# Optimization experiments

Hardware: AMD Instinct MI355X
Metric: run time of the kernel (lower is better)

Reference implementation:

```python
import jax, jax.numpy as jnp
import numpy as np

D_MODEL = 256
KSIZE = 16
EPS = 1e-5


def conv1d(x, w, b):
    # x: [B, C, N], w: [O, C, K], SAME padding over node axis
    y = jax.lax.conv_general_dilated(x, w, window_strides=(1,), padding='SAME',
                                     dimension_numbers=('NCH', 'OIH', 'NCH'))
    return y + b[None, :, None]


def layernorm(x, g, b):
    mu = jnp.mean(x, axis=-1, keepdims=True)
    var = jnp.mean(jnp.square(x - mu), axis=-1, keepdims=True)
    return (x - mu) * jax.lax.rsqrt(var + EPS) * g + b


def setup_inputs() -> dict:
    key = jax.random.key(0)
    ks = jax.random.split(key, 16)
    B, N, d, K = 4, 2048, D_MODEL, KSIZE
    conv_scale = 1.0 / np.sqrt(d * K)
    lin_scale = 1.0 / np.sqrt(d)
    return {
        'src': jax.random.normal(ks[0], (B, N, d), jnp.float32),
        'x_lst': jnp.zeros((B, N, N), jnp.float32),
        'adj': jax.random.randint(ks[1], (B, N, N), 0, 2, jnp.int32),
        'dis': jax.random.uniform(ks[2], (B, N, N), jnp.float32),
        'Wq': jax.random.normal(ks[3], (d, d, K), jnp.float32) * conv_scale,
        'bq': jnp.zeros((d,), jnp.float32),
        'Wk': jax.random.normal(ks[4], (d, d, K), jnp.float32) * conv_scale,
        'bk': jnp.zeros((d,), jnp.float32),
        'Wv': jax.random.normal(ks[5], (d, d, K), jnp.float32) * conv_scale,
        'bv': jnp.zeros((d,), jnp.float32),
        'W1': jax.random.normal(ks[6], (d, d), jnp.float32) * lin_scale,
        'b1': jnp.zeros((d,), jnp.float32),
        'W2': jax.random.normal(ks[7], (d, d), jnp.float32) * lin_scale,
        'b2': jnp.zeros((d,), jnp.float32),
        'W3': jax.random.normal(ks[8], (d, d), jnp.float32) * lin_scale,
        'b3': jnp.zeros((d,), jnp.float32),
        'g1': jnp.ones((d,), jnp.float32),
        'be1': jnp.zeros((d,), jnp.float32),
        'g2': jnp.ones((d,), jnp.float32),
        'be2': jnp.zeros((d,), jnp.float32),
    }


def reference(src, x_lst, adj, dis, Wq, bq, Wk, bk, Wv, bv,
              W1, b1, W2, b2, W3, b3, g1, be1, g2, be2):
    # ---- _ga_block: transpose to channel-major, graph attention ----
    x = jnp.swapaxes(src, -2, -1)                      # [B, d, N]
    q = conv1d(x, Wq, bq)                              # [B, d, N]
    k = conv1d(x, Wk, bk)
    v = conv1d(x, Wv, bv)
    scale = 1.0 / jnp.sqrt(jnp.asarray(D_MODEL, src.dtype))
    scores = jnp.einsum('bdn,bdm->bnm', q, k) * scale  # [B, N, N]
    scores = scores - dis                              # distance bias
    scores = jnp.where(adj > 0, scores, jnp.asarray(-1e9, scores.dtype))
    attn = jax.nn.softmax(scores, axis=-1)             # [B, N, N]
    x_lst_new = x_lst + attn                           # accumulated attention state
    out = jnp.einsum('bnm,bdm->bdn', attn, v)          # [B, d, N]
    x1 = jnp.swapaxes(out, -2, -1)                     # [B, N, d] (dropout = identity in eval)
    # ---- residual + norm1 ----
    h = layernorm(src + x1, g1, be1)
    # ---- 3-layer LeakyReLU MLP + residual + norm2 ----
    m = jax.nn.leaky_relu(h @ W1.T + b1)
    m = jax.nn.leaky_relu(m @ W2.T + b2)
    m = m @ W3.T + b3
    h = layernorm(h + m, g2, be2)
    return h, x_lst_new
```

## Files before the change

kernel.cpp:

```cpp
#include <hip/hip_runtime.h>
#include <stdint.h>

typedef _Float16 h16;
typedef _Float16 h8v __attribute__((ext_vector_type(8)));
typedef float    f4v __attribute__((ext_vector_type(4)));
typedef int      i4v __attribute__((ext_vector_type(4)));

#define NBATCH 4
#define NNODE  2048
#define DM     256
#define NPAD   2063

__device__ __forceinline__ void async16(const void* g, void* l) {
#if __has_builtin(__builtin_amdgcn_global_load_lds)
  __builtin_amdgcn_global_load_lds((__attribute__((address_space(1))) void*)g,
                                   (__attribute__((address_space(3))) void*)l, 16, 0, 0);
#else
  *(f4v*)l = *(const f4v*)g;
#endif
}

__device__ __forceinline__ void gemm_tile(
    const h16* Abase, int astride,
    const h16* Bbase, int bstride,
    h16* As, h16* Bs, f4v acc[4][4], int kiters)
{
  const int tid  = threadIdx.x;
  const int lane = tid & 63;
  const int wv   = tid >> 6;
  const int srow = tid >> 2;
  const int sch  = ((tid & 3) ^ ((tid >> 3) & 3)) * 8;
  const h16* gA0 = Abase + (long)srow * astride + sch;
  const h16* gA1 = Abase + (long)(srow + 64) * astride + sch;
  const h16* gB0 = Bbase + (long)srow * bstride + sch;
  const h16* gB1 = Bbase + (long)(srow + 64) * bstride + sch;
  h16* lA0 = As + tid * 8;
  h16* lA1 = As + 2048 + tid * 8;
  h16* lB0 = Bs + tid * 8;
  h16* lB1 = Bs + 2048 + tid * 8;
  const int swz = ((lane & 15) >> 1) & 3;
  const int qq  = ((lane >> 4) ^ swz) * 8;
  const int amr = ((wv & 1) * 64 + (lane & 15)) * 32 + qq;
  const int bnr = ((wv >> 1) * 64 + (lane & 15)) * 32 + qq;

  for (int kt = 0; kt < kiters; ++kt) {
    const int k0 = kt * 32;
    __syncthreads();
    async16(gA0 + k0, lA0);
    async16(gA1 + k0, lA1);
    async16(gB0 + k0, lB0);
    async16(gB1 + k0, lB1);
    asm volatile("s_waitcnt vmcnt(0)" ::: "memory");
    __syncthreads();
    h8v af[4], bf[4];
#pragma unroll
    for (int i = 0; i < 4; ++i) af[i] = *(const h8v*)(As + amr + i * (16 * 32));
#pragma unroll
    for (int j = 0; j < 4; ++j) bf[j] = *(const h8v*)(Bs + bnr + j * (16 * 32));
#pragma unroll
    for (int i = 0; i < 4; ++i)
#pragma unroll
      for (int j = 0; j < 4; ++j)
        acc[i][j] = __builtin_amdgcn_mfma_f32_16x16x32_f16(af[i], bf[j], acc[i][j], 0, 0, 0);
  }
}

__device__ __forceinline__ void zero_acc(f4v acc[4][4]) {
#pragma unroll
  for (int i = 0; i < 4; ++i)
#pragma unroll
    for (int j = 0; j < 4; ++j) {
      f4v z = {0.f, 0.f, 0.f, 0.f};
      acc[i][j] = z;
    }
}

__global__ void prep_src_kernel(const float* __restrict__ src, h16* __restrict__ Xpad) {
  int idx = blockIdx.x * 256 + threadIdx.x;
  int c = idx & 255;
  int row = idx >> 8;
  int b = row / NPAD;
  int n = row - b * NPAD;
  float v = 0.f;
  int ns = n - 7;
  if (ns >= 0 && ns < NNODE) v = src[((long)b * NNODE + ns) * DM + c];
  Xpad[idx] = (h16)v;
}

__global__ void prep_wconv_kernel(const float* __restrict__ Wq, const float* __restrict__ Wk,
                                  const float* __restrict__ Wv, h16* __restrict__ Wt) {
  int idx = blockIdx.x * 256 + threadIdx.x;
  int w = idx >> 20;
  int rem = idx & 1048575;
  int o = rem >> 12;
  int tc = rem & 4095;
  int t = tc >> 8;
  int c = tc & 255;
  const float* W = (w == 0) ? Wq : (w == 1) ? Wk : Wv;
  Wt[idx] = (h16)W[(o * 256 + c) * 16 + t];
}

__global__ void prep_wlin_kernel(const float* __restrict__ W1, const float* __restrict__ W2,
                                 const float* __restrict__ W3, h16* __restrict__ Wl) {
  int idx = blockIdx.x * 256 + threadIdx.x;
  int w = idx >> 16;
  int rem = idx & 65535;
  const float* W = (w == 0) ? W1 : (w == 1) ? W2 : W3;
  Wl[idx] = (h16)W[rem];
}

__global__ __launch_bounds__(256) void conv_gemm_kernel(
    const h16* __restrict__ Xpad, const h16* __restrict__ Wt,
    const float* __restrict__ bq, const float* __restrict__ bk, const float* __restrict__ bv,
    h16* __restrict__ Q, h16* __restrict__ Ko, h16* __restrict__ Vt)
{
  __shared__ __align__(16) h16 As[4096];
  __shared__ __align__(16) h16 Bs[4096];
  const int mt = blockIdx.x, ct = blockIdx.y, w = blockIdx.z;
  const int m0 = mt * 128;
  const int b = m0 >> 11, n0 = m0 & 2047;
  const h16* Abase = Xpad + ((long)(b * NPAD + n0)) * DM;
  const h16* Bbase = Wt + (long)w * (256 * 4096) + (long)ct * 128 * 4096;
  f4v acc[4][4];
  zero_acc(acc);
  gemm_tile(Abase, DM, Bbase, 4096, As, Bs, acc, 128);

  const float* bias = (w == 0) ? bq : (w == 1) ? bk : bv;
  const int lane = threadIdx.x & 63, wv = threadIdx.x >> 6;
  const int rbase = (wv & 1) * 64 + (lane >> 4) * 4;
  const int cbase = (wv >> 1) * 64 + (lane & 15);
#pragma unroll
  for (int j = 0; j < 4; ++j) {
    const int gc = ct * 128 + cbase + j * 16;
    const float bias_v = bias[gc];
#pragma unroll
    for (int i = 0; i < 4; ++i) {
#pragma unroll
      for (int e = 0; e < 4; ++e) {
        const int gr = m0 + rbase + i * 16 + e;
        const float v = acc[i][j][e] + bias_v;
        if (w == 2) {
          const int bb = gr >> 11, n = gr & 2047;
          Vt[((long)(bb * 256 + gc)) * 2048 + n] = (h16)v;
        } else {
          h16* dst = (w == 0) ? Q : Ko;
          dst[(long)gr * 256 + gc] = (h16)v;
        }
      }
    }
  }
}

__global__ __launch_bounds__(256) void scores_gemm_kernel(
    const h16* __restrict__ Q, const h16* __restrict__ Km, h16* __restrict__ Sh)
{
  __shared__ __align__(16) h16 As[4096];
  __shared__ __align__(16) h16 Bs[4096];
  const int nt = blockIdx.x, mt = blockIdx.y, b = blockIdx.z;
  const h16* Abase = Q + ((long)b * NNODE + nt * 128) * 256;
  const h16* Bbase = Km + ((long)b * NNODE + mt * 128) * 256;
  f4v acc[4][4];
  zero_acc(acc);
  gemm_tile(Abase, 256, Bbase, 256, As, Bs, acc, 8);

  const int lane = threadIdx.x & 63, wv = threadIdx.x >> 6;
  const int rbase = (wv & 1) * 64 + (lane >> 4) * 4;
  const int cbase = (wv >> 1) * 64 + (lane & 15);
  h16* Srow = Sh + (long)b * NNODE * NNODE;
#pragma unroll
  for (int i = 0; i < 4; ++i) {
#pragma unroll
    for (int e = 0; e < 4; ++e) {
      const long row = nt * 128 + rbase + i * 16 + e;
#pragma unroll
      for (int j = 0; j < 4; ++j) {
        const int col = mt * 128 + cbase + j * 16;
        Srow[row * 2048 + col] = (h16)(acc[i][j][e] * 0.0625f);
      }
    }
  }
}

__device__ __forceinline__ float wred_max(float v) {
#pragma unroll
  for (int off = 32; off > 0; off >>= 1) v = fmaxf(v, __shfl_xor(v, off, 64));
  return v;
}
__device__ __forceinline__ float wred_sum(float v) {
#pragma unroll
  for (int off = 32; off > 0; off >>= 1) v += __shfl_xor(v, off, 64);
  return v;
}

__global__ __launch_bounds__(256) void softmax_kernel(
    h16* __restrict__ Sh, const float* __restrict__ dis, const int* __restrict__ adj,
    const float* __restrict__ x_lst, float* __restrict__ out_x)
{
  const int r = blockIdx.x;
  const long ro = (long)r * 2048;
  const int tid = threadIdx.x, lane = tid & 63, wv = tid >> 6;
  const int j0 = tid * 8;
  __shared__ float wmax[4], wsum[4];

  h8v sv = *(const h8v*)(Sh + ro + j0);
  f4v d0 = *(const f4v*)(dis + ro + j0);
  f4v d1 = *(const f4v*)(dis + ro + j0 + 4);
  i4v a0 = *(const i4v*)(adj + ro + j0);
  i4v a1 = *(const i4v*)(adj + ro + j0 + 4);

  float s[8];
#pragma unroll
  for (int k = 0; k < 4; ++k) s[k]     = (a0[k] > 0) ? ((float)sv[k]     - d0[k]) : -1e9f;
#pragma unroll
  for (int k = 0; k < 4; ++k) s[k + 4] = (a1[k] > 0) ? ((float)sv[k + 4] - d1[k]) : -1e9f;

  float m = s[0];
#pragma unroll
  for (int k = 1; k < 8; ++k) m = fmaxf(m, s[k]);
  m = wred_max(m);
  if (lane == 0) wmax[wv] = m;
  __syncthreads();
  m = fmaxf(fmaxf(wmax[0], wmax[1]), fmaxf(wmax[2], wmax[3]));

  float p[8], ls = 0.f;
#pragma unroll
  for (int k = 0; k < 8; ++k) { p[k] = __expf(s[k] - m); ls += p[k]; }
  ls = wred_sum(ls);
  if (lane == 0) wsum[wv] = ls;
  __syncthreads();
  const float inv = 1.0f / (wsum[0] + wsum[1] + wsum[2] + wsum[3]);

  f4v x0 = *(const f4v*)(x_lst + ro + j0);
  f4v x1 = *(const f4v*)(x_lst + ro + j0 + 4);
  f4v o0, o1;
  h8v pv;
#pragma unroll
  for (int k = 0; k < 4; ++k) {
    const float a = p[k] * inv, bq = p[k + 4] * inv;
    o0[k] = x0[k] + a; o1[k] = x1[k] + bq;
    pv[k] = (h16)a; pv[k + 4] = (h16)bq;
  }
  *(f4v*)(out_x + ro + j0) = o0;
  *(f4v*)(out_x + ro + j0 + 4) = o1;
  *(h8v*)(Sh + ro + j0) = pv;
}

__global__ __launch_bounds__(256) void av_gemm_kernel(
    const h16* __restrict__ Attn, const h16* __restrict__ Vt, float* __restrict__ X1)
{
  __shared__ __align__(16) h16 As[4096];
  __shared__ __align__(16) h16 Bs[4096];
  const int nt = blockIdx.x, ct = blockIdx.y, b = blockIdx.z;
  const h16* Abase = Attn + ((long)b * NNODE + nt * 128) * 2048;
  const h16* Bbase = Vt + ((long)b * 256 + ct * 128) * 2048;
  f4v acc[4][4];
  zero_acc(acc);
  gemm_tile(Abase, 2048, Bbase, 2048, As, Bs, acc, 64);

  const int lane = threadIdx.x & 63, wv = threadIdx.x >> 6;
  const int rbase = (wv & 1) * 64 + (lane >> 4) * 4;
  const int cbase = (wv >> 1) * 64 + (lane & 15);
#pragma unroll
  for (int i = 0; i < 4; ++i) {
#pragma unroll
    for (int e = 0; e < 4; ++e) {
      const long row = (long)b * NNODE + nt * 128 + rbase + i * 16 + e;
#pragma unroll
      for (int j = 0; j < 4; ++j) {
        const int col = ct * 128 + cbase + j * 16;
        X1[row * 256 + col] = acc[i][j][e];
      }
    }
  }
}

__global__ __launch_bounds__(256) void mlp_gemm_kernel(
    const h16* __restrict__ A, const h16* __restrict__ W, const float* __restrict__ bias,
    h16* __restrict__ outH, float* __restrict__ outF)
{
  __shared__ __align__(16) h16 As[4096];
  __shared__ __align__(16) h16 Bs[4096];
  const int mt = blockIdx.x, ct = blockIdx.y;
  const h16* Abase = A + (long)mt * 128 * 256;
  const h16* Bbase = W + (long)ct * 128 * 256;
  f4v acc[4][4];
  zero_acc(acc);
  gemm_tile(Abase, 256, Bbase, 256, As, Bs, acc, 8);

  const int lane = threadIdx.x & 63, wv = threadIdx.x >> 6;
  const int rbase = (wv & 1) * 64 + (lane >> 4) * 4;
  const int cbase = (wv >> 1) * 64 + (lane & 15);
#pragma unroll
  for (int j = 0; j < 4; ++j) {
    const int gc = ct * 128 + cbase + j * 16;
    const float bias_v = bias[gc];
#pragma unroll
    for (int i = 0; i < 4; ++i) {
#pragma unroll
      for (int e = 0; e < 4; ++e) {
        const long gr = (long)mt * 128 + rbase + i * 16 + e;
        float v = acc[i][j][e] + bias_v;
        if (outH) {
          v = (v >= 0.f) ? v : 0.01f * v;
          outH[gr * 256 + gc] = (h16)v;
        } else {
          outF[gr * 256 + gc] = v;
        }
      }
    }
  }
}

__global__ __launch_bounds__(256) void ln_kernel(
    const float* __restrict__ X, const float* __restrict__ Y,
    const float* __restrict__ g, const float* __restrict__ bb,
    float* __restrict__ outF, h16* __restrict__ outH)
{
  const int wv = threadIdx.x >> 6, lane = threadIdx.x & 63;
  const long r = (long)blockIdx.x * 4 + wv;
  const long off = r * 256 + lane * 4;
  f4v x = *(const f4v*)(X + off);
  f4v y = *(const f4v*)(Y + off);
  float v[4];
  float sum = 0.f, sq = 0.f;
#pragma unroll
  for (int k = 0; k < 4; ++k) { v[k] = x[k] + y[k]; sum += v[k]; sq += v[k] * v[k]; }
  sum = wred_sum(sum);
  sq  = wred_sum(sq);
  const float mu = sum * (1.0f / 256.0f);
  const float var = sq * (1.0f / 256.0f) - mu * mu;
  const float rs = rsqrtf(var + 1e-5f);
  f4v gg = *(const f4v*)(g + lane * 4);
  f4v be = *(const f4v*)(bb + lane * 4);
  f4v o;
#pragma unroll
  for (int k = 0; k < 4; ++k) o[k] = (v[k] - mu) * rs * gg[k] + be[k];
  if (outF) *(f4v*)(outF + off) = o;
  if (outH) {
    _Float16 hv[4];
#pragma unroll
    for (int k = 0; k < 4; ++k) hv[k] = (h16)o[k];
    *(ulong1*)(outH + off) = *(ulong1*)hv;
  }
}

extern "C" void kernel_launch(void* const* d_in, const int* in_sizes, int n_in,
                              void* d_out, int out_size, void* d_ws, size_t ws_size,
                              hipStream_t stream)
{
  const float* src  = (const float*)d_in[0];
  const float* xlst = (const float*)d_in[1];
  const int*   adj  = (const int*)d_in[2];
  const float* dis  = (const float*)d_in[3];
  const float* Wq   = (const float*)d_in[4];
  const float* bq   = (const float*)d_in[5];
  const float* Wk   = (const float*)d_in[6];
  const float* bk   = (const float*)d_in[7];
  const float* Wv   = (const float*)d_in[8];
  const float* bvp  = (const float*)d_in[9];
  const float* W1   = (const float*)d_in[10];
  const float* b1   = (const float*)d_in[11];
  const float* W2   = (const float*)d_in[12];
  const float* b2   = (const float*)d_in[13];
  const float* W3   = (const float*)d_in[14];
  const float* b3   = (const float*)d_in[15];
  const float* g1   = (const float*)d_in[16];
  const float* be1  = (const float*)d_in[17];
  const float* g2   = (const float*)d_in[18];
  const float* be2  = (const float*)d_in[19];
  (void)in_sizes; (void)n_in; (void)out_size; (void)ws_size;

  char* ws = (char*)d_ws;
  size_t off = 0;
  auto alloc = [&](size_t bytes) -> void* {
    void* p = ws + off;
    off += (bytes + 1023) & ~(size_t)1023;
    return p;
  };
  h16*   Xpad = (h16*)  alloc((size_t)NBATCH * NPAD * DM * 2);
  h16*   Wt   = (h16*)  alloc((size_t)3 * 256 * 4096 * 2);
  h16*   Wl   = (h16*)  alloc((size_t)3 * 256 * 256 * 2);
  h16*   Qb   = (h16*)  alloc((size_t)NBATCH * NNODE * DM * 2);
  h16*   Kb   = (h16*)  alloc((size_t)NBATCH * NNODE * DM * 2);
  h16*   Vt   = (h16*)  alloc((size_t)NBATCH * DM * NNODE * 2);
  h16*   Sh   = (h16*)  alloc((size_t)NBATCH * NNODE * NNODE * 2);
  float* X1   = (float*)alloc((size_t)NBATCH * NNODE * DM * 4);
  float* H    = (float*)alloc((size_t)NBATCH * NNODE * DM * 4);
  h16*   H16  = (h16*)  alloc((size_t)NBATCH * NNODE * DM * 2);
  h16*   M1   = (h16*)  alloc((size_t)NBATCH * NNODE * DM * 2);
  h16*   M2   = (h16*)  alloc((size_t)NBATCH * NNODE * DM * 2);
  float* M3   = X1;

  float* out_h = (float*)d_out;
  float* out_x = out_h + (size_t)NBATCH * NNODE * DM;

  prep_src_kernel<<<(NBATCH * NPAD * DM) / 256, 256, 0, stream>>>(src, Xpad);
  prep_wconv_kernel<<<(3 * 256 * 4096) / 256, 256, 0, stream>>>(Wq, Wk, Wv, Wt);
  prep_wlin_kernel<<<(3 * 256 * 256) / 256, 256, 0, stream>>>(W1, W2, W3, Wl);

  conv_gemm_kernel<<<dim3(64, 2, 3), 256, 0, stream>>>(Xpad, Wt, bq, bk, bvp, Qb, Kb, Vt);
  scores_gemm_kernel<<<dim3(16, 16, 4), 256, 0, stream>>>(Qb, Kb, Sh);
  softmax_kernel<<<NBATCH * NNODE, 256, 0, stream>>>(Sh, dis, adj, xlst, out_x);
  av_gemm_kernel<<<dim3(16, 2, 4), 256, 0, stream>>>(Sh, Vt, X1);
  ln_kernel<<<(NBATCH * NNODE) / 4, 256, 0, stream>>>(src, X1, g1, be1, H, H16);
  mlp_gemm_kernel<<<dim3(64, 2), 256, 0, stream>>>(H16, Wl, b1, M1, nullptr);
  mlp_gemm_kernel<<<dim3(64, 2), 256, 0, stream>>>(M1, Wl + 65536, b2, M2, nullptr);
  mlp_gemm_kernel<<<dim3(64, 2), 256, 0, stream>>>(M2, Wl + 2 * 65536, b3, nullptr, M3);
  ln_kernel<<<(NBATCH * NNODE) / 4, 256, 0, stream>>>(H, M3, g2, be2, out_h, nullptr);
}
```

Measured before the change: 481.8 us.

## Double-buffer GEMM LDS tiles and split-K the attention-value GEMM

The shared GEMM tile loop now double-buffers its LDS tiles: it prefetches the next K-slice with async global-to-LDS loads while the MFMAs run on the current slice, which also removes one barrier per iteration. Every GEMM kernel doubles its LDS arrays to hold the two buffers. Separately, the attention-times-V GEMM is split into two K halves, doubling its grid from 128 to 256 blocks for better CU occupancy. The two partial sums go to separate buffers and are added inside the first layernorm. The cost is more LDS per block, which may lower occupancy, plus extra traffic to write and read the second fp32 partial buffer.

```diff
diff --git a/kernel.cpp b/kernel.cpp
--- a/kernel.cpp
+++ b/kernel.cpp
@@ -10,6 +10,7 @@
 #define NNODE  2048
 #define DM     256
 #define NPAD   2063
+#define PARTN  (8192 * 256)
 
 __device__ __forceinline__ void async16(const void* g, void* l) {
 #if __has_builtin(__builtin_amdgcn_global_load_lds)
@@ -43,20 +44,24 @@
   const int amr = ((wv & 1) * 64 + (lane & 15)) * 32 + qq;
   const int bnr = ((wv >> 1) * 64 + (lane & 15)) * 32 + qq;
 
+  async16(gA0, lA0); async16(gA1, lA1);
+  async16(gB0, lB0); async16(gB1, lB1);
+
   for (int kt = 0; kt < kiters; ++kt) {
-    const int k0 = kt * 32;
-    __syncthreads();
-    async16(gA0 + k0, lA0);
-    async16(gA1 + k0, lA1);
-    async16(gB0 + k0, lB0);
-    async16(gB1 + k0, lB1);
     asm volatile("s_waitcnt vmcnt(0)" ::: "memory");
     __syncthreads();
+    const int cur = (kt & 1) << 12;
+    if (kt + 1 < kiters) {
+      const int nxt = (~kt & 1) << 12;
+      const int k0 = (kt + 1) * 32;
+      async16(gA0 + k0, lA0 + nxt); async16(gA1 + k0, lA1 + nxt);
+      async16(gB0 + k0, lB0 + nxt); async16(gB1 + k0, lB1 + nxt);
+    }
     h8v af[4], bf[4];
 #pragma unroll
-    for (int i = 0; i < 4; ++i) af[i] = *(const h8v*)(As + amr + i * (16 * 32));
-#pragma unroll
-    for (int j = 0; j < 4; ++j) bf[j] = *(const h8v*)(Bs + bnr + j * (16 * 32));
+    for (int i = 0; i < 4; ++i) af[i] = *(const h8v*)(As + cur + amr + i * 512);
+#pragma unroll
+    for (int j = 0; j < 4; ++j) bf[j] = *(const h8v*)(Bs + cur + bnr + j * 512);
 #pragma unroll
     for (int i = 0; i < 4; ++i)
 #pragma unroll
@@ -114,8 +119,8 @@
     const float* __restrict__ bq, const float* __restrict__ bk, const float* __restrict__ bv,
     h16* __restrict__ Q, h16* __restrict__ Ko, h16* __restrict__ Vt)
 {
-  __shared__ __align__(16) h16 As[4096];
-  __shared__ __align__(16) h16 Bs[4096];
+  __shared__ __align__(16) h16 As[8192];
+  __shared__ __align__(16) h16 Bs[8192];
   const int mt = blockIdx.x, ct = blockIdx.y, w = blockIdx.z;
   const int m0 = mt * 128;
   const int b = m0 >> 11, n0 = m0 & 2047;
@@ -154,8 +159,8 @@
 __global__ __launch_bounds__(256) void scores_gemm_kernel(
     const h16* __restrict__ Q, const h16* __restrict__ Km, h16* __restrict__ Sh)
 {
-  __shared__ __align__(16) h16 As[4096];
-  __shared__ __align__(16) h16 Bs[4096];
+  __shared__ __align__(16) h16 As[8192];
+  __shared__ __align__(16) h16 Bs[8192];
   const int nt = blockIdx.x, mt = blockIdx.y, b = blockIdx.z;
   const h16* Abase = Q + ((long)b * NNODE + nt * 128) * 256;
   const h16* Bbase = Km + ((long)b * NNODE + mt * 128) * 256;
@@ -246,20 +251,22 @@
 }
 
 __global__ __launch_bounds__(256) void av_gemm_kernel(
-    const h16* __restrict__ Attn, const h16* __restrict__ Vt, float* __restrict__ X1)
-{
-  __shared__ __align__(16) h16 As[4096];
-  __shared__ __align__(16) h16 Bs[4096];
-  const int nt = blockIdx.x, ct = blockIdx.y, b = blockIdx.z;
-  const h16* Abase = Attn + ((long)b * NNODE + nt * 128) * 2048;
-  const h16* Bbase = Vt + ((long)b * 256 + ct * 128) * 2048;
+    const h16* __restrict__ Attn, const h16* __restrict__ Vt, float* __restrict__ X1p)
+{
+  __shared__ __align__(16) h16 As[8192];
+  __shared__ __align__(16) h16 Bs[8192];
+  const int nt = blockIdx.x, b = blockIdx.z;
+  const int ct = blockIdx.y & 1, ks = blockIdx.y >> 1;
+  const h16* Abase = Attn + ((long)b * NNODE + nt * 128) * 2048 + ks * 1024;
+  const h16* Bbase = Vt + ((long)b * 256 + ct * 128) * 2048 + ks * 1024;
   f4v acc[4][4];
   zero_acc(acc);
-  gemm_tile(Abase, 2048, Bbase, 2048, As, Bs, acc, 64);
+  gemm_tile(Abase, 2048, Bbase, 2048, As, Bs, acc, 32);
 
   const int lane = threadIdx.x & 63, wv = threadIdx.x >> 6;
   const int rbase = (wv & 1) * 64 + (lane >> 4) * 4;
   const int cbase = (wv >> 1) * 64 + (lane & 15);
+  float* dst = X1p + (long)ks * PARTN;
 #pragma unroll
   for (int i = 0; i < 4; ++i) {
 #pragma unroll
@@ -268,7 +275,7 @@
 #pragma unroll
       for (int j = 0; j < 4; ++j) {
         const int col = ct * 128 + cbase + j * 16;
-        X1[row * 256 + col] = acc[i][j][e];
+        dst[row * 256 + col] = acc[i][j][e];
       }
     }
   }
@@ -278,8 +285,8 @@
     const h16* __restrict__ A, const h16* __restrict__ W, const float* __restrict__ bias,
     h16* __restrict__ outH, float* __restrict__ outF)
 {
-  __shared__ __align__(16) h16 As[4096];
-  __shared__ __align__(16) h16 Bs[4096];
+  __shared__ __align__(16) h16 As[8192];
+  __shared__ __align__(16) h16 Bs[8192];
   const int mt = blockIdx.x, ct = blockIdx.y;
   const h16* Abase = A + (long)mt * 128 * 256;
   const h16* Bbase = W + (long)ct * 128 * 256;
@@ -312,7 +319,7 @@
 }
 
 __global__ __launch_bounds__(256) void ln_kernel(
-    const float* __restrict__ X, const float* __restrict__ Y,
+    const float* __restrict__ X, const float* __restrict__ Y, const float* __restrict__ Y2,
     const float* __restrict__ g, const float* __restrict__ bb,
     float* __restrict__ outF, h16* __restrict__ outH)
 {
@@ -321,6 +328,11 @@
   const long off = r * 256 + lane * 4;
   f4v x = *(const f4v*)(X + off);
   f4v y = *(const f4v*)(Y + off);
+  if (Y2) {
+    f4v y2 = *(const f4v*)(Y2 + off);
+#pragma unroll
+    for (int k = 0; k < 4; ++k) y[k] += y2[k];
+  }
   float v[4];
   float sum = 0.f, sq = 0.f;
 #pragma unroll
@@ -384,12 +396,12 @@
   h16*   Kb   = (h16*)  alloc((size_t)NBATCH * NNODE * DM * 2);
   h16*   Vt   = (h16*)  alloc((size_t)NBATCH * DM * NNODE * 2);
   h16*   Sh   = (h16*)  alloc((size_t)NBATCH * NNODE * NNODE * 2);
-  float* X1   = (float*)alloc((size_t)NBATCH * NNODE * DM * 4);
+  float* X1p  = (float*)alloc((size_t)2 * PARTN * 4);
   float* H    = (float*)alloc((size_t)NBATCH * NNODE * DM * 4);
   h16*   H16  = (h16*)  alloc((size_t)NBATCH * NNODE * DM * 2);
   h16*   M1   = (h16*)  alloc((size_t)NBATCH * NNODE * DM * 2);
   h16*   M2   = (h16*)  alloc((size_t)NBATCH * NNODE * DM * 2);
-  float* M3   = X1;
+  float* M3   = X1p;
 
   float* out_h = (float*)d_out;
   float* out_x = out_h + (size_t)NBATCH * NNODE * DM;
@@ -401,10 +413,10 @@
   conv_gemm_kernel<<<dim3(64, 2, 3), 256, 0, stream>>>(Xpad, Wt, bq, bk, bvp, Qb, Kb, Vt);
   scores_gemm_kernel<<<dim3(16, 16, 4), 256, 0, stream>>>(Qb, Kb, Sh);
   softmax_kernel<<<NBATCH * NNODE, 256, 0, stream>>>(Sh, dis, adj, xlst, out_x);
-  av_gemm_kernel<<<dim3(16, 2, 4), 256, 0, stream>>>(Sh, Vt, X1);
-  ln_kernel<<<(NBATCH * NNODE) / 4, 256, 0, stream>>>(src, X1, g1, be1, H, H16);
+  av_gemm_kernel<<<dim3(16, 4, 4), 256, 0, stream>>>(Sh, Vt, X1p);
+  ln_kernel<<<(NBATCH * NNODE) / 4, 256, 0, stream>>>(src, X1p, X1p + PARTN, g1, be1, H, H16);
   mlp_gemm_kernel<<<dim3(64, 2), 256, 0, stream>>>(H16, Wl, b1, M1, nullptr);
   mlp_gemm_kernel<<<dim3(64, 2), 256, 0, stream>>>(M1, Wl + 65536, b2, M2, nullptr);
   mlp_gemm_kernel<<<dim3(64, 2), 256, 0, stream>>>(M2, Wl + 2 * 65536, b3, nullptr, M3);
-  ln_kernel<<<(NBATCH * NNODE) / 4, 256, 0, stream>>>(H, M3, g2, be2, out_h, nullptr);
-}
+  ln_kernel<<<(NBATCH * NNODE) / 4, 256, 0, stream>>>(H, M3, nullptr, g2, be2, out_h, nullptr);
+}
```

Measured after the change: 482.1 us. About the same (+0.1%).
